# Optimization experiments

Hardware: AMD Instinct MI355X
Metric: run time of the kernel (lower is better)

## Reference

```python
import jax, jax.numpy as jnp
import numpy as np

N_NODES = 50000
N_GRAPHS = 64
IN_DIM, HIDDEN, OUT_DIM = 2063, 256, 128
E_L, E_G = 800000, 1600000


def setup_inputs() -> dict:
    key = jax.random.key(0)
    ks = jax.random.split(key, 16)
    x = jax.random.normal(ks[0], (N_NODES, IN_DIM), dtype=jnp.float32)
    edge_index_l = jax.random.randint(ks[1], (2, E_L), 0, N_NODES, dtype=jnp.int64)
    edge_index_g = jax.random.randint(ks[2], (2, E_G), 0, N_NODES, dtype=jnp.int64)
    batch = jnp.sort(jax.random.randint(ks[3], (N_NODES,), 0, N_GRAPHS, dtype=jnp.int64))

    def glorot(k, shape):
        scale = jnp.sqrt(2.0 / (shape[0] + shape[1])).astype(jnp.float32)
        return jax.random.normal(k, shape, dtype=jnp.float32) * scale

    return {
        "x": x,
        "edge_index_l": edge_index_l,
        "edge_index_g": edge_index_g,
        "batch": batch,
        "W_l1": glorot(ks[4], (IN_DIM, HIDDEN)), "b_l1": jnp.zeros((HIDDEN,), jnp.float32),
        "W_l2": glorot(ks[5], (HIDDEN, OUT_DIM)), "b_l2": jnp.zeros((OUT_DIM,), jnp.float32),
        "W_g1": glorot(ks[6], (IN_DIM, HIDDEN)), "b_g1": jnp.zeros((HIDDEN,), jnp.float32),
        "W_g2": glorot(ks[7], (HIDDEN, OUT_DIM)), "b_g2": jnp.zeros((OUT_DIM,), jnp.float32),
        "W_fuse": glorot(ks[8], (2 * OUT_DIM, OUT_DIM)), "b_fuse": jnp.zeros((OUT_DIM,), jnp.float32),
    }


def gcn_conv(x, edge_index, W, b):
    # PyG GCNConv: add self loops, symmetric D^{-1/2}(A+I)D^{-1/2} normalization,
    # linear transform then scatter-add aggregation at target nodes.
    n = x.shape[0]
    loops = jnp.arange(n, dtype=edge_index.dtype)
    src = jnp.concatenate([edge_index[0], loops])
    dst = jnp.concatenate([edge_index[1], loops])
    deg = jax.ops.segment_sum(jnp.ones_like(dst, dtype=x.dtype), dst, num_segments=n)
    dinv = jax.lax.rsqrt(deg)  # deg >= 1 due to self loops
    norm = dinv[src] * dinv[dst]  # [E+n]
    h = x @ W  # [n, out]
    msg = h[src] * norm[:, None]  # gather + scale
    return jax.ops.segment_sum(msg, dst, num_segments=n) + b


def global_mean_pool(x, batch, num_graphs):
    sums = jax.ops.segment_sum(x, batch, num_segments=num_graphs)
    cnt = jax.ops.segment_sum(jnp.ones((x.shape[0],), x.dtype), batch, num_segments=num_graphs)
    return sums / jnp.maximum(cnt, 1.0)[:, None]


def reference(x, edge_index_l, edge_index_g, batch,
              W_l1, b_l1, W_l2, b_l2, W_g1, b_g1, W_g2, b_g2, W_fuse, b_fuse):
    # dropout is identity in eval mode
    xl = jax.nn.relu(gcn_conv(x, edge_index_l, W_l1, b_l1))
    xl = gcn_conv(xl, edge_index_l, W_l2, b_l2)
    xl = global_mean_pool(xl, batch, N_GRAPHS)

    xg = jax.nn.relu(gcn_conv(x, edge_index_g, W_g1, b_g1))
    xg = gcn_conv(xg, edge_index_g, W_g2, b_g2)
    xg = global_mean_pool(xg, batch, N_GRAPHS)

    out = jnp.concatenate([xl, xg], axis=1)  # [G, 2*out_dim]
    return jax.nn.relu(out @ W_fuse + b_fuse)
```

## Files before the change

kernel.cpp:

```cpp
#include <hip/hip_runtime.h>
#include <hip/hip_bf16.h>
#include <cstdint>
#include <cstddef>


#define N_NODES 50000
#define N_GRAPHS 64
#define IN_DIM 2063
#define HIDDEN 256
#define OUT_DIM 128
#define EDGES_L 800000
#define EDGES_G 1600000
#define HCOLS 512
#define KPAD 2112
#define MPAD 50048
#define GBM 64
#define PCH 256
#define NCHUNK ((N_NODES + PCH - 1) / PCH)

#define QUARTER 12544
#define SL_L 64
#define SL_G 128
#define EPS 12500
#define HBLOCKS (4 * (SL_L + SL_G))

typedef __attribute__((ext_vector_type(8))) __bf16 bf16x8;
typedef __attribute__((ext_vector_type(4))) float f32x4;

__device__ __forceinline__ float bf2f(unsigned short u) {
  union { unsigned int i; float f; } c; c.i = ((unsigned int)u) << 16; return c.f;
}
__device__ __forceinline__ unsigned short f2bf(float f) {
  __hip_bfloat16 h = __float2bfloat16(f);
  return *reinterpret_cast<unsigned short*>(&h);
}

__global__ void k_cvt_w(const float* __restrict__ Wl, const float* __restrict__ Wg,
                        unsigned short* __restrict__ Wt) {
  int i = blockIdx.x * blockDim.x + threadIdx.x;
  if (i >= HCOLS * KPAD) return;
  int n = i / KPAD;
  int k = i - n * KPAD;
  float v = 0.f;
  if (k < IN_DIM) {
    v = (n < HIDDEN) ? Wl[(size_t)k * HIDDEN + n] : Wg[(size_t)k * HIDDEN + (n - HIDDEN)];
  }
  Wt[(size_t)n * KPAD + k] = f2bf(v);
}

__launch_bounds__(256)
__global__ void k_hist(const int* __restrict__ dstL, const int* __restrict__ dstG,
                       int* __restrict__ partL, int* __restrict__ partG) {
  __shared__ int hist[QUARTER];
  const int i = blockIdx.x;
  const int* __restrict__ dst;
  int slice, q;
  int* __restrict__ part;
  if (i < 4 * SL_L) {
    slice = i >> 2; q = i & 3;
    dst = dstL;
    part = partL + (size_t)(slice * 4 + q) * QUARTER;
  } else {
    int j = i - 4 * SL_L;
    slice = j >> 2; q = j & 3;
    dst = dstG;
    part = partG + (size_t)(slice * 4 + q) * QUARTER;
  }
  for (int t = threadIdx.x; t < QUARTER; t += 256) hist[t] = 0;
  __syncthreads();
  const int e0 = slice * EPS;
  const int qbase = q * QUARTER;
  for (int e = e0 + threadIdx.x; e < e0 + EPS; e += 256) {
    int d = dst[e] - qbase;
    if ((unsigned)d < QUARTER) atomicAdd(&hist[d], 1);
  }
  __syncthreads();
  for (int t = threadIdx.x; t < QUARTER; t += 256) part[t] = hist[t];
}

__global__ void k_prefix(int* __restrict__ partL, int* __restrict__ partG,
                         const int* __restrict__ batch, int* __restrict__ degL,
                         int* __restrict__ degG, float* __restrict__ dinvL,
                         float* __restrict__ dinvG, float* __restrict__ cL,
                         float* __restrict__ cG) {
  int t = blockIdx.x * blockDim.x + threadIdx.x;
  if (t >= 8 * QUARTER) return;
  const int b = t / (4 * QUARTER);
  const int n = t - b * 4 * QUARTER;
  const int q = n / QUARTER, loc = n - q * QUARTER;
  const int NS = b ? SL_G : SL_L;
  int* p = (b ? partG : partL) + (size_t)q * QUARTER + loc;
  int run = 0;
  for (int s = 0; s < NS; s++) {
    int* pp = p + (size_t)s * 4 * QUARTER;
    int v = *pp;
    *pp = run;
    run += v;
  }
  if (n < N_NODES) {
    float d = 1.0f / sqrtf((float)(run + 1));
    if (b == 0) {
      degL[n] = run; dinvL[n] = d; cL[(size_t)n * 64 + batch[n]] = d * d;
    } else {
      degG[n] = run; dinvG[n] = d; cG[(size_t)n * 64 + batch[n]] = d * d;
    }
  }
}

__global__ void k_scan1(const int* __restrict__ degL, const int* __restrict__ degG,
                        int* __restrict__ rowL, int* __restrict__ rowG,
                        const int* __restrict__ batch, int* __restrict__ start) {
  if (blockIdx.x >= 2) {
    int n = (blockIdx.x - 2) * 1024 + threadIdx.x;
    if (n >= N_NODES) return;
    int bn = batch[n];
    int bp = n ? batch[n - 1] : -1;
    for (int g = bp + 1; g <= bn; g++) start[g] = n;
    if (n == N_NODES - 1)
      for (int g = bn + 1; g <= N_GRAPHS; g++) start[g] = N_NODES;
    return;
  }
  __shared__ int part[1024];
  const int t = threadIdx.x;
  const int* __restrict__ deg = blockIdx.x ? degG : degL;
  int* __restrict__ row = blockIdx.x ? rowG : rowL;
  const int c0 = t * 49;
  int s = 0;
  for (int j = 0; j < 49; j++) {
    int idx = c0 + j;
    s += (idx < N_NODES) ? deg[idx] : 0;
  }
  part[t] = s;
  __syncthreads();
  for (int ofs = 1; ofs < 1024; ofs <<= 1) {
    int v = (t >= ofs) ? part[t - ofs] : 0;
    __syncthreads();
    part[t] += v;
    __syncthreads();
  }
  int run = (t > 0) ? part[t - 1] : 0;
  for (int j = 0; j < 49; j++) {
    int idx = c0 + j;
    if (idx < N_NODES) { row[idx] = run; run += deg[idx]; }
  }
  if (t == 1023) row[N_NODES] = part[1023];
}

__launch_bounds__(256)
__global__ void k_scatter2(const int* __restrict__ srcL, const int* __restrict__ dstL,
                           const int* __restrict__ srcG, const int* __restrict__ dstG,
                           const int* __restrict__ partL, const int* __restrict__ partG,
                           const int* __restrict__ rowL, const int* __restrict__ rowG,
                           const float* __restrict__ dinvL, const float* __restrict__ dinvG,
                           const int* __restrict__ batch, int2* __restrict__ erL,
                           int2* __restrict__ erG, float* __restrict__ cL,
                           float* __restrict__ cG) {
  __shared__ int hist[QUARTER];
  const int i = blockIdx.x;
  const int *src, *dst, *part, *row;
  const float* dinv;
  int2* er;
  float* c;
  int slice, q;
  if (i < 4 * SL_L) {
    slice = i >> 2; q = i & 3;
    src = srcL; dst = dstL; row = rowL; dinv = dinvL; er = erL; c = cL;
    part = partL + (size_t)(slice * 4 + q) * QUARTER;
  } else {
    int j = i - 4 * SL_L;
    slice = j >> 2; q = j & 3;
    src = srcG; dst = dstG; row = rowG; dinv = dinvG; er = erG; c = cG;
    part = partG + (size_t)(slice * 4 + q) * QUARTER;
  }
  for (int t = threadIdx.x; t < QUARTER; t += 256) hist[t] = 0;
  __syncthreads();
  const int e0 = slice * EPS;
  const int qbase = q * QUARTER;
  for (int e = e0 + threadIdx.x; e < e0 + EPS; e += 256) {
    int d = dst[e];
    int loc = d - qbase;
    if ((unsigned)loc < QUARTER) {
      int s = src[e];
      int rank = atomicAdd(&hist[loc], 1);
      int pos = row[d] + part[loc] + rank;
      float nrm = dinv[s] * dinv[d];
      er[pos] = make_int2(s, __float_as_int(nrm));
      atomicAdd(&c[(size_t)s * 64 + batch[d]], nrm);
    }
  }
}

__launch_bounds__(256, 2)
__global__ void k_mfma_gemm(const float* __restrict__ X,
                            const unsigned short* __restrict__ Wt,
                            unsigned short* __restrict__ H) {
  __shared__ __align__(16) char lds[8192 + 65536];
  const int tid = threadIdx.x;
  const int lane = tid & 63;
  const int wave = tid >> 6;
  const int brow = blockIdx.x * GBM;

  const int ar = tid >> 2;
  const int ak = (tid & 3) * 16;
  const int arow_g = brow + ar;
  const bool aok = arow_g < N_NODES;
  const float* __restrict__ Arow = X + (size_t)arow_g * IN_DIM;
  const int ac0 = (tid & 3) * 2;
  char* const awr0 = lds + ar * 128 + ((ac0 ^ (ar & 7)) * 16);
  char* const awr1 = lds + ar * 128 + (((ac0 + 1) ^ (ar & 7)) * 16);

  const int fr = lane & 15;
  const int fq = lane >> 4;

  f32x4 acc[4][8];
  const f32x4 zero = {0.f, 0.f, 0.f, 0.f};
#pragma unroll
  for (int m = 0; m < 4; m++)
#pragma unroll
    for (int n = 0; n < 8; n++) acc[m][n] = zero;

  float a[16];
#pragma unroll
  for (int j = 0; j < 16; j++) a[j] = aok ? Arow[ak + j] : 0.f;

  for (int t = 0; t < KPAD / 64; ++t) {
    const int k0 = t * 64;
#pragma unroll
    for (int i = 0; i < 16; i++) {
      const int s = i * 256 + wave * 64 + lane;
      const int row = s >> 3, cch = s & 7;
      const unsigned short* g = Wt + (size_t)row * KPAD + k0 + ((cch ^ (row & 7)) * 8);
      __builtin_amdgcn_global_load_lds(
          (const __attribute__((address_space(1))) void*)g,
          (__attribute__((address_space(3))) void*)(lds + 8192 + (i * 256 + wave * 64) * 16),
          16, 0, 0);
    }
    {
      uint u0 = (uint)f2bf(a[0]) | ((uint)f2bf(a[1]) << 16);
      uint u1 = (uint)f2bf(a[2]) | ((uint)f2bf(a[3]) << 16);
      uint u2 = (uint)f2bf(a[4]) | ((uint)f2bf(a[5]) << 16);
      uint u3 = (uint)f2bf(a[6]) | ((uint)f2bf(a[7]) << 16);
      uint u4 = (uint)f2bf(a[8]) | ((uint)f2bf(a[9]) << 16);
      uint u5 = (uint)f2bf(a[10]) | ((uint)f2bf(a[11]) << 16);
      uint u6 = (uint)f2bf(a[12]) | ((uint)f2bf(a[13]) << 16);
      uint u7 = (uint)f2bf(a[14]) | ((uint)f2bf(a[15]) << 16);
      *(uint4*)awr0 = make_uint4(u0, u1, u2, u3);
      *(uint4*)awr1 = make_uint4(u4, u5, u6, u7);
    }
    __syncthreads();

    if (t + 1 < KPAD / 64) {
      const int kb = k0 + 64 + ak;
      if (aok) {
        if (kb + 15 < IN_DIM) {
#pragma unroll
          for (int j = 0; j < 16; j++) a[j] = Arow[kb + j];
        } else {
#pragma unroll
          for (int j = 0; j < 16; j++) a[j] = (kb + j < IN_DIM) ? Arow[kb + j] : 0.f;
        }
      }
    }

#pragma unroll
    for (int kk = 0; kk < 2; kk++) {
      const int kc = kk * 4 + fq;
      bf16x8 bv[8];
#pragma unroll
      for (int n = 0; n < 8; n++) {
        const int row = wave * 128 + n * 16 + fr;
        bv[n] = *(const bf16x8*)(lds + 8192 + row * 128 + ((kc ^ (row & 7)) * 16));
      }
#pragma unroll
      for (int m = 0; m < 4; m++) {
        const int row = m * 16 + fr;
        bf16x8 av = *(const bf16x8*)(lds + row * 128 + ((kc ^ (row & 7)) * 16));
#pragma unroll
        for (int n = 0; n < 8; n++)
          acc[m][n] = __builtin_amdgcn_mfma_f32_16x16x32_bf16(av, bv[n], acc[m][n], 0, 0, 0);
      }
    }
    __syncthreads();
  }

#pragma unroll
  for (int m = 0; m < 4; m++) {
    const int r0 = brow + m * 16 + fq * 4;
#pragma unroll
    for (int n = 0; n < 8; n++) {
      const int col = wave * 128 + n * 16 + fr;
#pragma unroll
      for (int j = 0; j < 4; j++) {
        int r = r0 + j;
        if (r < N_NODES) H[(size_t)r * HCOLS + col] = f2bf(acc[m][n][j]);
      }
    }
  }
}

__global__ void k_agg(const unsigned short* __restrict__ h,
                      const float* __restrict__ dinvL, const float* __restrict__ dinvG,
                      const int* __restrict__ rowL, const int* __restrict__ rowG,
                      const int2* __restrict__ erL, const int2* __restrict__ erG,
                      const float* __restrict__ biasL, const float* __restrict__ biasG,
                      unsigned short* __restrict__ xl) {
  const int br = blockIdx.y;
  const int node = blockIdx.x * 4 + (threadIdx.x >> 6);
  const int lane = threadIdx.x & 63;
  const float* __restrict__ dinv = br ? dinvG : dinvL;
  const int* __restrict__ rp = br ? rowG : rowL;
  const int2* __restrict__ er = br ? erG : erL;
  const float* __restrict__ bias = br ? biasG : biasL;
  const int off = br ? 256 : 0;
  const size_t lcol = off + lane * 4;

  float di = dinv[node];
  float w0 = di * di;
  ushort4 u = *(const ushort4*)(h + (size_t)node * HCOLS + lcol);
  float a0 = w0 * bf2f(u.x), a1 = w0 * bf2f(u.y), a2 = w0 * bf2f(u.z), a3 = w0 * bf2f(u.w);

  int e = rp[node];
  const int e1 = rp[node + 1];
  for (; e + 8 <= e1; e += 8) {
    int2 r[8];
    ushort4 v[8];
#pragma unroll
    for (int j = 0; j < 8; j++) r[j] = er[e + j];
#pragma unroll
    for (int j = 0; j < 8; j++)
      v[j] = *(const ushort4*)(h + (size_t)r[j].x * HCOLS + lcol);
#pragma unroll
    for (int j = 0; j < 8; j++) {
      float w = __int_as_float(r[j].y);
      a0 = fmaf(w, bf2f(v[j].x), a0);
      a1 = fmaf(w, bf2f(v[j].y), a1);
      a2 = fmaf(w, bf2f(v[j].z), a2);
      a3 = fmaf(w, bf2f(v[j].w), a3);
    }
  }
  for (; e + 4 <= e1; e += 4) {
    int2 r[4];
    ushort4 v[4];
#pragma unroll
    for (int j = 0; j < 4; j++) r[j] = er[e + j];
#pragma unroll
    for (int j = 0; j < 4; j++)
      v[j] = *(const ushort4*)(h + (size_t)r[j].x * HCOLS + lcol);
#pragma unroll
    for (int j = 0; j < 4; j++) {
      float w = __int_as_float(r[j].y);
      a0 = fmaf(w, bf2f(v[j].x), a0);
      a1 = fmaf(w, bf2f(v[j].y), a1);
      a2 = fmaf(w, bf2f(v[j].z), a2);
      a3 = fmaf(w, bf2f(v[j].w), a3);
    }
  }
  for (; e < e1; e++) {
    int2 r = er[e];
    float w = __int_as_float(r.y);
    ushort4 v = *(const ushort4*)(h + (size_t)r.x * HCOLS + lcol);
    a0 = fmaf(w, bf2f(v.x), a0);
    a1 = fmaf(w, bf2f(v.y), a1);
    a2 = fmaf(w, bf2f(v.z), a2);
    a3 = fmaf(w, bf2f(v.w), a3);
  }
  float4 b = *(const float4*)(bias + lane * 4);
  ushort4 o;
  o.x = f2bf(fmaxf(a0 + b.x, 0.f));
  o.y = f2bf(fmaxf(a1 + b.y, 0.f));
  o.z = f2bf(fmaxf(a2 + b.z, 0.f));
  o.w = f2bf(fmaxf(a3 + b.w, 0.f));
  *(ushort4*)(xl + (size_t)node * HCOLS + lcol) = o;
}

__launch_bounds__(256)
__global__ void k_pool2(const unsigned short* __restrict__ xl,
                        const float* __restrict__ cL, const float* __restrict__ cG,
                        float* __restrict__ Spart) {
  __shared__ float cs[64][64];
  const int t = threadIdx.x;
  const int chunk = blockIdx.x;
  const int br = blockIdx.y;
  const float* __restrict__ C = br ? cG : cL;
  const int xoff = br ? 256 : 0;
  const int n0 = chunk * PCH;
  float acc[64];
#pragma unroll
  for (int g = 0; g < 64; g++) acc[g] = 0.f;

  for (int tile = 0; tile < PCH; tile += 64) {
    const int base = n0 + tile;
    __syncthreads();
#pragma unroll
    for (int i = 0; i < 16; i++) {
      int idx = i * 256 + t;
      int nn = idx >> 6, gg = idx & 63;
      int node = base + nn;
      cs[nn][gg] = (node < N_NODES) ? C[(size_t)node * 64 + gg] : 0.f;
    }
    __syncthreads();
    for (int nn = 0; nn < 64; nn++) {
      int node = base + nn;
      float v = (node < N_NODES) ? bf2f(xl[(size_t)node * HCOLS + xoff + t]) : 0.f;
#pragma unroll
      for (int g4 = 0; g4 < 16; g4++) {
        float4 cv = *(const float4*)&cs[nn][g4 * 4];
        acc[g4 * 4 + 0] = fmaf(cv.x, v, acc[g4 * 4 + 0]);
        acc[g4 * 4 + 1] = fmaf(cv.y, v, acc[g4 * 4 + 1]);
        acc[g4 * 4 + 2] = fmaf(cv.z, v, acc[g4 * 4 + 2]);
        acc[g4 * 4 + 3] = fmaf(cv.w, v, acc[g4 * 4 + 3]);
      }
    }
  }
  float* sp = Spart + ((size_t)br * NCHUNK + chunk) * 16384 + t;
#pragma unroll
  for (int g = 0; g < 64; g++) sp[g * 256] = acc[g];
}

__global__ void k_pool_reduce(const float* __restrict__ Spart, float* __restrict__ S) {
  int i = blockIdx.x * blockDim.x + threadIdx.x;
  if (i >= 2 * 16384) return;
  int br = i >> 14, idx = i & 16383;
  const float* p = Spart + (size_t)br * NCHUNK * 16384 + idx;
  float s = 0.f;
  for (int ch = 0; ch < NCHUNK; ch++) s += p[(size_t)ch * 16384];
  S[i] = s;
}

__global__ void k_final(const float* __restrict__ S,
                        const float* __restrict__ Wl2, const float* __restrict__ bl2,
                        const float* __restrict__ Wg2, const float* __restrict__ bg2,
                        const float* __restrict__ Wf, const float* __restrict__ bf,
                        const int* __restrict__ start, float* __restrict__ out) {
  __shared__ float pl[OUT_DIM], pg[OUT_DIM];
  int g = blockIdx.x, t = threadIdx.x;
  float invc = 1.0f / fmaxf((float)(start[g + 1] - start[g]), 1.0f);
  const float* Sl = S + (size_t)g * HIDDEN;
  const float* Sg = S + (size_t)N_GRAPHS * HIDDEN + (size_t)g * HIDDEN;
  float al = 0.f, ag = 0.f;
  for (int k = 0; k < HIDDEN; k++) {
    al = fmaf(Sl[k], Wl2[k * OUT_DIM + t], al);
    ag = fmaf(Sg[k], Wg2[k * OUT_DIM + t], ag);
  }
  pl[t] = al * invc + bl2[t];
  pg[t] = ag * invc + bg2[t];
  __syncthreads();
  float o = bf[t];
  for (int j = 0; j < OUT_DIM; j++) {
    o = fmaf(pl[j], Wf[j * OUT_DIM + t], o);
    o = fmaf(pg[j], Wf[(OUT_DIM + j) * OUT_DIM + t], o);
  }
  out[(size_t)g * OUT_DIM + t] = fmaxf(o, 0.f);
}

extern "C" void kernel_launch(void* const* d_in, const int* in_sizes, int n_in,
                              void* d_out, int out_size, void* d_ws, size_t ws_size,
                              hipStream_t stream) {
  const float* x = (const float*)d_in[0];
  const int* el = (const int*)d_in[1];
  const int* eg = (const int*)d_in[2];
  const int* batch = (const int*)d_in[3];
  const float* Wl1 = (const float*)d_in[4];
  const float* bl1 = (const float*)d_in[5];
  const float* Wl2 = (const float*)d_in[6];
  const float* bl2 = (const float*)d_in[7];
  const float* Wg1 = (const float*)d_in[8];
  const float* bg1 = (const float*)d_in[9];
  const float* Wg2 = (const float*)d_in[10];
  const float* bg2 = (const float*)d_in[11];
  const float* Wf = (const float*)d_in[12];
  const float* bf = (const float*)d_in[13];
  float* out = (float*)d_out;
  char* ws = (char*)d_ws;

  const size_t NPAD = 200192;
  size_t off = 0;
  float* c_l = (float*)(ws + off); off += (size_t)N_NODES * 64 * 4;
  float* c_g = (float*)(ws + off); off += (size_t)N_NODES * 64 * 4;
  const size_t zero_bytes = off;
  int* start = (int*)(ws + off); off += 512;
  float* S = (float*)(ws + off); off += (size_t)2 * N_GRAPHS * HIDDEN * 4;
  int* deg_l = (int*)(ws + off); off += NPAD;
  int* deg_g = (int*)(ws + off); off += NPAD;
  float* dinv_l = (float*)(ws + off); off += NPAD;
  float* dinv_g = (float*)(ws + off); off += NPAD;
  int* row_l = (int*)(ws + off); off += NPAD;
  int* row_g = (int*)(ws + off); off += NPAD;
  int* partL = (int*)(ws + off); off += (size_t)SL_L * 4 * QUARTER * 4;
  int* partG = (int*)(ws + off); off += (size_t)SL_G * 4 * QUARTER * 4;
  int2* er_l = (int2*)(ws + off); off += (size_t)EDGES_L * 8;
  int2* er_g = (int2*)(ws + off); off += (size_t)EDGES_G * 8;
  unsigned short* Wt = (unsigned short*)(ws + off); off += (size_t)HCOLS * KPAD * 2;
  unsigned short* h = (unsigned short*)(ws + off); off += (size_t)N_NODES * HCOLS * 2;
  unsigned short* xl = (unsigned short*)(ws + off); off += (size_t)N_NODES * HCOLS * 2;
  float* Spart = (float*)partL;

  const int* srcL = el;
  const int* dstL = el + EDGES_L;
  const int* srcG = eg;
  const int* dstG = eg + EDGES_G;

  hipMemsetAsync(ws, 0, zero_bytes, stream);

  k_cvt_w<<<(HCOLS * KPAD + 255) / 256, 256, 0, stream>>>(Wl1, Wg1, Wt);

  k_hist<<<HBLOCKS, 256, 0, stream>>>(dstL, dstG, partL, partG);
  k_prefix<<<(8 * QUARTER + 255) / 256, 256, 0, stream>>>(partL, partG, batch, deg_l, deg_g,
                                                          dinv_l, dinv_g, c_l, c_g);
  k_scan1<<<51, 1024, 0, stream>>>(deg_l, deg_g, row_l, row_g, batch, start);
  k_scatter2<<<HBLOCKS, 256, 0, stream>>>(srcL, dstL, srcG, dstG, partL, partG, row_l, row_g,
                                          dinv_l, dinv_g, batch, er_l, er_g, c_l, c_g);

  k_mfma_gemm<<<MPAD / GBM, 256, 0, stream>>>(x, Wt, h);

  dim3 agrid(N_NODES / 4, 2);
  k_agg<<<agrid, 256, 0, stream>>>(h, dinv_l, dinv_g, row_l, row_g, er_l, er_g, bl1, bg1, xl);

  dim3 pgrid(NCHUNK, 2);
  k_pool2<<<pgrid, 256, 0, stream>>>(xl, c_l, c_g, Spart);
  k_pool_reduce<<<(2 * 16384 + 255) / 256, 256, 0, stream>>>(Spart, S);

  k_final<<<N_GRAPHS, OUT_DIM, 0, stream>>>(S, Wl2, bl2, Wg2, bg2, Wf, bf, start, out);
}
```

Measured before the change: 958.8 us.

## Read GEMM weights directly from global and double-buffer the A tile in LDS

The dense GEMM kernel no longer stages the 64 KB weight tile in LDS through global_load_lds. Each wave now reads its B fragments straight from global memory (the weights are small and likely cache-resident), and the A tile goes into a double-buffered 16 KB LDS area, so each iteration needs one barrier instead of two. The much smaller LDS footprint and the relaxed launch bounds are meant to raise occupancy and overlap loads with MFMA work. The cost is uncoalesced per-lane 16-byte global reads of B that depend on L2/MALL hits, plus exposed global latency right before the MFMAs.

```diff
diff --git a/kernel.cpp b/kernel.cpp
--- a/kernel.cpp
+++ b/kernel.cpp
@@ -190,11 +190,11 @@
   }
 }
 
-__launch_bounds__(256, 2)
+__launch_bounds__(256)
 __global__ void k_mfma_gemm(const float* __restrict__ X,
                             const unsigned short* __restrict__ Wt,
                             unsigned short* __restrict__ H) {
-  __shared__ __align__(16) char lds[8192 + 65536];
+  __shared__ __align__(16) char lds[2][8192];
   const int tid = threadIdx.x;
   const int lane = tid & 63;
   const int wave = tid >> 6;
@@ -206,8 +206,8 @@
   const bool aok = arow_g < N_NODES;
   const float* __restrict__ Arow = X + (size_t)arow_g * IN_DIM;
   const int ac0 = (tid & 3) * 2;
-  char* const awr0 = lds + ar * 128 + ((ac0 ^ (ar & 7)) * 16);
-  char* const awr1 = lds + ar * 128 + (((ac0 + 1) ^ (ar & 7)) * 16);
+  const int aw0 = ar * 128 + ((ac0 ^ (ar & 7)) * 16);
+  const int aw1 = ar * 128 + (((ac0 + 1) ^ (ar & 7)) * 16);
 
   const int fr = lane & 15;
   const int fq = lane >> 4;
@@ -222,20 +222,57 @@
   float a[16];
 #pragma unroll
   for (int j = 0; j < 16; j++) a[j] = aok ? Arow[ak + j] : 0.f;
+  {
+    uint u0 = (uint)f2bf(a[0]) | ((uint)f2bf(a[1]) << 16);
+    uint u1 = (uint)f2bf(a[2]) | ((uint)f2bf(a[3]) << 16);
+    uint u2 = (uint)f2bf(a[4]) | ((uint)f2bf(a[5]) << 16);
+    uint u3 = (uint)f2bf(a[6]) | ((uint)f2bf(a[7]) << 16);
+    uint u4 = (uint)f2bf(a[8]) | ((uint)f2bf(a[9]) << 16);
+    uint u5 = (uint)f2bf(a[10]) | ((uint)f2bf(a[11]) << 16);
+    uint u6 = (uint)f2bf(a[12]) | ((uint)f2bf(a[13]) << 16);
+    uint u7 = (uint)f2bf(a[14]) | ((uint)f2bf(a[15]) << 16);
+    *(uint4*)(lds[0] + aw0) = make_uint4(u0, u1, u2, u3);
+    *(uint4*)(lds[0] + aw1) = make_uint4(u4, u5, u6, u7);
+  }
+  __syncthreads();
 
   for (int t = 0; t < KPAD / 64; ++t) {
     const int k0 = t * 64;
-#pragma unroll
-    for (int i = 0; i < 16; i++) {
-      const int s = i * 256 + wave * 64 + lane;
-      const int row = s >> 3, cch = s & 7;
-      const unsigned short* g = Wt + (size_t)row * KPAD + k0 + ((cch ^ (row & 7)) * 8);
-      __builtin_amdgcn_global_load_lds(
-          (const __attribute__((address_space(1))) void*)g,
-          (__attribute__((address_space(3))) void*)(lds + 8192 + (i * 256 + wave * 64) * 16),
-          16, 0, 0);
-    }
-    {
+    const int cur = t & 1;
+
+    if (t + 1 < KPAD / 64) {
+      const int kb = k0 + 64 + ak;
+      if (aok) {
+        if (kb + 15 < IN_DIM) {
+#pragma unroll
+          for (int j = 0; j < 16; j++) a[j] = Arow[kb + j];
+        } else {
+#pragma unroll
+          for (int j = 0; j < 16; j++) a[j] = (kb + j < IN_DIM) ? Arow[kb + j] : 0.f;
+        }
+      }
+    }
+
+#pragma unroll
+    for (int kk = 0; kk < 2; kk++) {
+      const int kc = kk * 4 + fq;
+      bf16x8 bv[8];
+#pragma unroll
+      for (int n = 0; n < 8; n++) {
+        const int row = wave * 128 + n * 16 + fr;
+        bv[n] = *(const bf16x8*)(Wt + (size_t)row * KPAD + k0 + kc * 8);
+      }
+#pragma unroll
+      for (int m = 0; m < 4; m++) {
+        const int row = m * 16 + fr;
+        bf16x8 av = *(const bf16x8*)(lds[cur] + row * 128 + ((kc ^ (row & 7)) * 16));
+#pragma unroll
+        for (int n = 0; n < 8; n++)
+          acc[m][n] = __builtin_amdgcn_mfma_f32_16x16x32_bf16(av, bv[n], acc[m][n], 0, 0, 0);
+      }
+    }
+
+    if (t + 1 < KPAD / 64) {
       uint u0 = (uint)f2bf(a[0]) | ((uint)f2bf(a[1]) << 16);
       uint u1 = (uint)f2bf(a[2]) | ((uint)f2bf(a[3]) << 16);
       uint u2 = (uint)f2bf(a[4]) | ((uint)f2bf(a[5]) << 16);
@@ -244,43 +281,11 @@
       uint u5 = (uint)f2bf(a[10]) | ((uint)f2bf(a[11]) << 16);
       uint u6 = (uint)f2bf(a[12]) | ((uint)f2bf(a[13]) << 16);
       uint u7 = (uint)f2bf(a[14]) | ((uint)f2bf(a[15]) << 16);
-      *(uint4*)awr0 = make_uint4(u0, u1, u2, u3);
-      *(uint4*)awr1 = make_uint4(u4, u5, u6, u7);
-    }
-    __syncthreads();
-
-    if (t + 1 < KPAD / 64) {
-      const int kb = k0 + 64 + ak;
-      if (aok) {
-        if (kb + 15 < IN_DIM) {
-#pragma unroll
-          for (int j = 0; j < 16; j++) a[j] = Arow[kb + j];
-        } else {
-#pragma unroll
-          for (int j = 0; j < 16; j++) a[j] = (kb + j < IN_DIM) ? Arow[kb + j] : 0.f;
-        }
-      }
-    }
-
-#pragma unroll
-    for (int kk = 0; kk < 2; kk++) {
-      const int kc = kk * 4 + fq;
-      bf16x8 bv[8];
-#pragma unroll
-      for (int n = 0; n < 8; n++) {
-        const int row = wave * 128 + n * 16 + fr;
-        bv[n] = *(const bf16x8*)(lds + 8192 + row * 128 + ((kc ^ (row & 7)) * 16));
-      }
-#pragma unroll
-      for (int m = 0; m < 4; m++) {
-        const int row = m * 16 + fr;
-        bf16x8 av = *(const bf16x8*)(lds + row * 128 + ((kc ^ (row & 7)) * 16));
-#pragma unroll
-        for (int n = 0; n < 8; n++)
-          acc[m][n] = __builtin_amdgcn_mfma_f32_16x16x32_bf16(av, bv[n], acc[m][n], 0, 0, 0);
-      }
-    }
-    __syncthreads();
+      char* wb = lds[cur ^ 1];
+      *(uint4*)(wb + aw0) = make_uint4(u0, u1, u2, u3);
+      *(uint4*)(wb + aw1) = make_uint4(u4, u5, u6, u7);
+      __syncthreads();
+    }
   }
 
 #pragma unroll
```

After: 1.175 ms. 22.6% more time.
